# Optimization experiments

Hardware: AMD Instinct MI355X
Metric: run time of the kernel (lower is better)

Reference implementation:

```python
import jax, jax.numpy as jnp
import numpy as np

B, T, C = 2, 2048, 1024
N_HEAD = 16
HEAD_DIM = C // N_HEAD


def setup_inputs() -> dict:
    key = jax.random.key(0)
    k1, k2, k3, k4, k5 = jax.random.split(key, 5)
    s = 1.0 / np.sqrt(C)
    return {
        "x": jax.random.normal(k1, (B, T, C), dtype=jnp.float32),
        "w_attn": jax.random.normal(k2, (C, 3 * C), dtype=jnp.float32) * s,
        "b_attn": jax.random.normal(k3, (3 * C,), dtype=jnp.float32) * 0.02,
        "w_proj": jax.random.normal(k4, (C, C), dtype=jnp.float32) * s,
        "b_proj": jax.random.normal(k5, (C,), dtype=jnp.float32) * 0.02,
    }


def reference(x, w_attn, b_attn, w_proj, b_proj):
    Bx, Tx, Cx = x.shape
    qkv = x @ w_attn + b_attn  # [B, T, 3C]
    q, k, v = jnp.split(qkv, 3, axis=2)
    # [B, H, T, D]
    q = q.reshape(Bx, Tx, N_HEAD, HEAD_DIM).transpose(0, 2, 1, 3)
    k = k.reshape(Bx, Tx, N_HEAD, HEAD_DIM).transpose(0, 2, 1, 3)
    v = v.reshape(Bx, Tx, N_HEAD, HEAD_DIM).transpose(0, 2, 1, 3)
    scale = 1.0 / jnp.sqrt(jnp.asarray(HEAD_DIM, dtype=x.dtype))
    att = jnp.einsum("bhqd,bhkd->bhqk", q, k) * scale  # [B,H,T,T]
    causal = jnp.tril(jnp.ones((Tx, Tx), dtype=bool))
    att = jnp.where(causal[None, None, :, :], att, -jnp.inf)
    att = jax.nn.softmax(att, axis=-1)
    y = jnp.einsum("bhqk,bhkd->bhqd", att, v)  # [B,H,T,D]
    y = y.transpose(0, 2, 1, 3).reshape(Bx, Tx, Cx)
    return y @ w_proj + b_proj
```

## Files before the change

kernel.cpp:

```cpp
#include <hip/hip_runtime.h>
#include <hip/hip_bf16.h>
#include <stdint.h>

#define TT 2048
#define CC 1024
#define NH 16
#define HD 64
#define BT 4096

typedef float f32x4 __attribute__((ext_vector_type(4)));
typedef __bf16 bf16x8 __attribute__((ext_vector_type(8)));
typedef __bf16 bf16x4 __attribute__((ext_vector_type(4)));
typedef short sh4 __attribute__((ext_vector_type(4)));

#define MFMA(a, b, c) __builtin_amdgcn_mfma_f32_16x16x32_bf16((a), (b), (c), 0, 0, 0)
#define MFMA16(a, b, c) __builtin_amdgcn_mfma_f32_16x16x16bf16_1k((a), (b), (c), 0, 0, 0)

__device__ __forceinline__ void gload16(const void* g, void* l) {
    __builtin_amdgcn_global_load_lds(
        (const __attribute__((address_space(1))) void*)g,
        (__attribute__((address_space(3))) void*)l,
        16, 0, 0);
}

__global__ __launch_bounds__(256) void prep(
    const float* __restrict__ x, __bf16* __restrict__ xb,
    const float* __restrict__ wa, __bf16* __restrict__ oa,
    const float* __restrict__ wp, __bf16* __restrict__ op) {
    __shared__ float tile[32][33];
    int b0 = blockIdx.x;
    if (b0 < 1024) {
        int i = b0 * 256 + threadIdx.x;
        const int stride = 1024 * 256;
        const int n4 = BT * CC / 4;
        for (; i < n4; i += stride) {
            float4 v = reinterpret_cast<const float4*>(x)[i];
            bf16x4 o;
            o.x = (__bf16)v.x; o.y = (__bf16)v.y;
            o.z = (__bf16)v.z; o.w = (__bf16)v.w;
            reinterpret_cast<bf16x4*>(xb)[i] = o;
        }
    } else {
        int idx = b0 - 1024;
        int bx = idx & 127, r0 = (idx >> 7) * 32;
        const float* in;
        __bf16* out;
        int C;
        if (bx < 96) { in = wa; out = oa; C = 3072; }
        else         { in = wp; out = op; C = 1024; bx -= 96; }
        int c0 = bx * 32;
        int tx = threadIdx.x & 31, ty = (threadIdx.x >> 5) & 7;
#pragma unroll
        for (int j = 0; j < 32; j += 8)
            tile[ty + j][tx] = in[(size_t)(r0 + ty + j) * C + c0 + tx];
        __syncthreads();
#pragma unroll
        for (int j = 0; j < 32; j += 8)
            out[(size_t)(c0 + ty + j) * 1024 + r0 + tx] = (__bf16)tile[tx][ty + j];
    }
}

template <int MODE, int XPX>
__global__ __launch_bounds__(256) void gemm128(
    const __bf16* __restrict__ A, const __bf16* __restrict__ Bt,
    const float* __restrict__ bias,
    __bf16* __restrict__ oq, __bf16* __restrict__ ok, __bf16* __restrict__ ov,
    float* __restrict__ of, int M, int N, int K) {
    __shared__ __align__(16) __bf16 As[128 * 64];
    __shared__ __align__(16) __bf16 Bs[128 * 64];
    const int tid = threadIdx.x;
    const int w = tid >> 6, lane = tid & 63;
    const int l15 = lane & 15, lg = lane >> 4;
    const int id = blockIdx.x;
    const int jx = id & 7, s = id >> 3;
    const int xcol = jx * XPX + (s % XPX);
    const int yrow = s / XPX;
    const int m0 = yrow * 128, n0 = xcol * 128;
    const int wr = w >> 1, wc = w & 1;

    const f32x4 zero4 = {0.f, 0.f, 0.f, 0.f};
    f32x4 acc[4][4];
#pragma unroll
    for (int m = 0; m < 4; ++m)
#pragma unroll
        for (int n = 0; n < 4; ++n) acc[m][n] = zero4;

    const char* Ab = (const char*)A;
    const char* Bb = (const char*)Bt;
    const size_t rowbytes = (size_t)K * 2;

    for (int kt = 0; kt < K; kt += 64) {
#pragma unroll
        for (int j = 0; j < 4; ++j) {
            int base = (w * 4 + j) * 1024;
            int d0 = base + lane * 16;
            int row = d0 >> 7;
            int colb = d0 & 127;
            int scolb = colb ^ ((row & 7) << 4);
            gload16(Ab + (size_t)(m0 + row) * rowbytes + (size_t)kt * 2 + scolb,
                    (char*)As + base);
            gload16(Bb + (size_t)(n0 + row) * rowbytes + (size_t)kt * 2 + scolb,
                    (char*)Bs + base);
        }
        __syncthreads();
#pragma unroll
        for (int kk = 0; kk < 2; ++kk) {
            bf16x8 af[4], bfr[4];
#pragma unroll
            for (int m = 0; m < 4; ++m) {
                int row = wr * 64 + m * 16 + l15;
                int colb = kk * 64 + lg * 16;
                af[m] = *(const bf16x8*)((const char*)As + row * 128 +
                                         (colb ^ ((row & 7) << 4)));
            }
#pragma unroll
            for (int n = 0; n < 4; ++n) {
                int row = wc * 64 + n * 16 + l15;
                int colb = kk * 64 + lg * 16;
                bfr[n] = *(const bf16x8*)((const char*)Bs + row * 128 +
                                          (colb ^ ((row & 7) << 4)));
            }
#pragma unroll
            for (int m = 0; m < 4; ++m)
#pragma unroll
                for (int n = 0; n < 4; ++n)
                    acc[m][n] = MFMA(af[m], bfr[n], acc[m][n]);
        }
        __syncthreads();
    }

#pragma unroll
    for (int n = 0; n < 4; ++n) {
        int col = n0 + wc * 64 + n * 16 + l15;
        float bs = bias[col];
        if constexpr (MODE == 0) {
            int sec = col >> 10;
            int cc = col & 1023;
            int h = cc >> 6, d = cc & 63;
            if (sec == 2) {
#pragma unroll
                for (int m = 0; m < 4; ++m) {
                    int rowb = m0 + wr * 64 + m * 16 + lg * 4;
                    int bb = rowb >> 11, t = rowb & 2047;
                    bf16x4 pk;
#pragma unroll
                    for (int r = 0; r < 4; ++r) pk[r] = (__bf16)(acc[m][n][r] + bs);
                    size_t base = ((size_t)(bb * NH + h) * HD + d) * (TT * 2);
                    size_t byte = base + (size_t)((t & ~63) * 2 +
                                   (((t & 63) * 2) ^ ((d & 15) << 3)));
                    *(bf16x4*)((char*)ov + byte) = pk;
                }
            } else {
                __bf16* dst = (sec == 0) ? oq : ok;
                float mult = (sec == 0) ? 0.125f * 1.44269504088896340736f : 1.0f;
#pragma unroll
                for (int m = 0; m < 4; ++m) {
                    int rowb = m0 + wr * 64 + m * 16 + lg * 4;
#pragma unroll
                    for (int r = 0; r < 4; ++r) {
                        int row = rowb + r;
                        int bb = row >> 11, t = row & 2047;
                        float val = (acc[m][n][r] + bs) * mult;
                        dst[((size_t)(bb * NH + h) * TT + t) * HD + d] = (__bf16)val;
                    }
                }
            }
        } else {
#pragma unroll
            for (int m = 0; m < 4; ++m) {
                int rowb = m0 + wr * 64 + m * 16 + lg * 4;
#pragma unroll
                for (int r = 0; r < 4; ++r) {
                    int row = rowb + r;
                    of[(size_t)row * N + col] = acc[m][n][r] + bs;
                }
            }
        }
    }
}

__global__ __launch_bounds__(256) void attn_kernel(
    const __bf16* __restrict__ q, const __bf16* __restrict__ k,
    const __bf16* __restrict__ vt, __bf16* __restrict__ y) {
    __shared__ __align__(16) __bf16 Kb[2][64 * 64];
    __shared__ __align__(16) __bf16 Vb[2][64 * 64];

    const int n = blockIdx.x;
    const int batch = n >> 8, a = (n >> 5) & 7;
    const int qt = (batch == 0) ? 31 - a : (batch == 1) ? 16 + a
                 : (batch == 2) ? 15 - a : a;
    const int bh = ((n & 7) << 2) | ((n >> 3) & 3);
    const int tid = threadIdx.x, w = tid >> 6, lane = tid & 63;
    const int l15 = lane & 15, lg = lane >> 4;
    const char* kh = (const char*)(k + (size_t)bh * TT * HD);
    const char* vh = (const char*)(vt + (size_t)bh * HD * TT);
    const __bf16* qh = q + (size_t)bh * TT * HD;
    const int qbw = qt * 64 + w * 16;

    const f32x4 zero4 = {0.f, 0.f, 0.f, 0.f};
    float lrun = 0.f;
    f32x4 oacc[4];
    bf16x8 qf[2];
#pragma unroll
    for (int f = 0; f < 4; ++f) oacc[f] = zero4;
#pragma unroll
    for (int kk = 0; kk < 2; ++kk)
        qf[kk] = *(const bf16x8*)&qh[(size_t)(qbw + l15) * HD + kk * 32 + lg * 8];

    auto stage = [&](int kvb, int buf) {
#pragma unroll
        for (int j = 0; j < 2; ++j) {
            int d0 = ((w * 2 + j) * 64 + lane) * 16;
            int row = d0 >> 7, colb = d0 & 127;
            gload16(kh + (size_t)(kvb + row) * 128 + (colb ^ ((row & 7) << 4)),
                    (char*)Kb[buf] + d0);
            gload16(vh + (size_t)row * (TT * 2) + (size_t)kvb * 2 + colb,
                    (char*)Vb[buf] + d0);
        }
    };

    stage(0, 0);
    __syncthreads();

    for (int g = 0; g <= qt; ++g) {
        const int cur = g & 1;
        if (g < qt) stage((g + 1) * 64, cur ^ 1);
        const int kb = g * 64;

        f32x4 s[4];
#pragma unroll
        for (int kf = 0; kf < 4; ++kf) s[kf] = zero4;
        __builtin_amdgcn_s_setprio(1);
#pragma unroll
        for (int kf = 0; kf < 4; ++kf) {
            int krow = kf * 16 + l15;
            const char* kr = (const char*)Kb[cur] + krow * 128;
            bf16x8 k0 = *(const bf16x8*)(kr + ((lg * 16) ^ ((krow & 7) << 4)));
            bf16x8 k1 = *(const bf16x8*)(kr + ((64 + lg * 16) ^ ((krow & 7) << 4)));
            s[kf] = MFMA(k0, qf[0], s[kf]);
            s[kf] = MFMA(k1, qf[1], s[kf]);
        }
        __builtin_amdgcn_s_setprio(0);
        if (g == qt) {
            const int qq = qbw + l15;
#pragma unroll
            for (int kf = 0; kf < 4; ++kf)
#pragma unroll
                for (int r = 0; r < 4; ++r) {
                    int kk_ = kb + kf * 16 + lg * 4 + r;
                    if (kk_ > qq) s[kf][r] = -1e30f;
                }
        }
        float ss = 0.f;
        sh4 pb[4];
#pragma unroll
        for (int kf = 0; kf < 4; ++kf) {
            bf16x4 pk;
#pragma unroll
            for (int r = 0; r < 4; ++r) {
                float p = exp2f(s[kf][r]);
                pk[r] = (__bf16)p;
                ss += p;
            }
            pb[kf] = __builtin_bit_cast(sh4, pk);
        }
        lrun += ss;
        __builtin_amdgcn_s_setprio(1);
#pragma unroll
        for (int kf = 0; kf < 4; ++kf) {
            int cb = (kf * 32 + lg * 8) ^ (l15 << 3);
#pragma unroll
            for (int f = 0; f < 4; ++f) {
                int vrow = f * 16 + l15;
                bf16x4 va = *(const bf16x4*)((const char*)Vb[cur] + vrow * 128 + cb);
                oacc[f] = MFMA16(__builtin_bit_cast(sh4, va), pb[kf], oacc[f]);
            }
        }
        __builtin_amdgcn_s_setprio(0);
        __syncthreads();
    }

    lrun += __shfl_xor(lrun, 16);
    lrun += __shfl_xor(lrun, 32);
    const int b = bh >> 4, h = bh & 15;
    float inv = 1.0f / lrun;
#pragma unroll
    for (int f = 0; f < 4; ++f) {
        bf16x4 pk;
#pragma unroll
        for (int r = 0; r < 4; ++r) pk[r] = (__bf16)(oacc[f][r] * inv);
        *(bf16x4*)&y[(size_t)(b * TT + qbw + l15) * CC + h * 64 + f * 16 +
                     lg * 4] = pk;
    }
}

extern "C" void kernel_launch(void* const* d_in, const int* in_sizes, int n_in,
                              void* d_out, int out_size, void* d_ws, size_t ws_size,
                              hipStream_t stream) {
    const float* x      = (const float*)d_in[0];
    const float* w_attn = (const float*)d_in[1];
    const float* b_attn = (const float*)d_in[2];
    const float* w_proj = (const float*)d_in[3];
    const float* b_proj = (const float*)d_in[4];
    float* out = (float*)d_out;

    char* ws = (char*)d_ws;
    size_t off = 0;
    auto alloc = [&](size_t bytes) {
        char* p = ws + off;
        off += (bytes + 255) & ~(size_t)255;
        return p;
    };
    __bf16* xb   = (__bf16*)alloc((size_t)BT * CC * 2);
    __bf16* watb = (__bf16*)alloc((size_t)3 * CC * CC * 2);
    __bf16* wptb = (__bf16*)alloc((size_t)CC * CC * 2);
    __bf16* qb   = (__bf16*)alloc((size_t)BT * CC * 2);
    __bf16* kbuf = (__bf16*)alloc((size_t)BT * CC * 2);
    __bf16* vtb  = (__bf16*)alloc((size_t)BT * CC * 2);
    __bf16* yb   = (__bf16*)alloc((size_t)BT * CC * 2);

    prep<<<5120, 256, 0, stream>>>(x, xb, w_attn, watb, w_proj, wptb);

    gemm128<0, 3><<<768, 256, 0, stream>>>(
        xb, watb, b_attn, qb, kbuf, vtb, nullptr, BT, 3 * CC, CC);

    attn_kernel<<<1024, 256, 0, stream>>>(qb, kbuf, vtb, yb);

    gemm128<1, 1><<<256, 256, 0, stream>>>(
        yb, wptb, b_proj, nullptr, nullptr, nullptr, out, BT, CC, CC);
}
```

Baseline: 109.1 us.

## Pair complementary causal query tiles per attention block to share K/V loads

Each attention workgroup now handles two query tiles (qt and 31-qt) of the same head, sharing the staged K/V tiles for the overlapping prefix. The grid halves to 512 blocks and every block does a balanced amount of causal work. This is meant to cut redundant K/V global and LDS traffic and remove load imbalance. In exchange it doubles accumulator register use, which may lower occupancy, and leaves fewer blocks to fill the GPU.

```diff
diff --git a/kernel.cpp b/kernel.cpp
--- a/kernel.cpp
+++ b/kernel.cpp
@@ -186,31 +186,34 @@
     __shared__ __align__(16) __bf16 Vb[2][64 * 64];
 
     const int n = blockIdx.x;
-    const int batch = n >> 8, a = (n >> 5) & 7;
-    const int qt = (batch == 0) ? 31 - a : (batch == 1) ? 16 + a
-                 : (batch == 2) ? 15 - a : a;
+    const int sl = (n >> 5) & 7;
+    const int j = (n < 256) ? (15 - sl) : sl;
+    const int qtA = 15 - j, qtB = 16 + j;
     const int bh = ((n & 7) << 2) | ((n >> 3) & 3);
     const int tid = threadIdx.x, w = tid >> 6, lane = tid & 63;
     const int l15 = lane & 15, lg = lane >> 4;
     const char* kh = (const char*)(k + (size_t)bh * TT * HD);
     const char* vh = (const char*)(vt + (size_t)bh * HD * TT);
     const __bf16* qh = q + (size_t)bh * TT * HD;
-    const int qbw = qt * 64 + w * 16;
+    const int qbwA = qtA * 64 + w * 16;
+    const int qbwB = qtB * 64 + w * 16;
 
     const f32x4 zero4 = {0.f, 0.f, 0.f, 0.f};
-    float lrun = 0.f;
-    f32x4 oacc[4];
-    bf16x8 qf[2];
-#pragma unroll
-    for (int f = 0; f < 4; ++f) oacc[f] = zero4;
-#pragma unroll
-    for (int kk = 0; kk < 2; ++kk)
-        qf[kk] = *(const bf16x8*)&qh[(size_t)(qbw + l15) * HD + kk * 32 + lg * 8];
+    float lrunA = 0.f, lrunB = 0.f;
+    f32x4 oaccA[4], oaccB[4];
+    bf16x8 qfA[2], qfB[2];
+#pragma unroll
+    for (int f = 0; f < 4; ++f) { oaccA[f] = zero4; oaccB[f] = zero4; }
+#pragma unroll
+    for (int kk = 0; kk < 2; ++kk) {
+        qfA[kk] = *(const bf16x8*)&qh[(size_t)(qbwA + l15) * HD + kk * 32 + lg * 8];
+        qfB[kk] = *(const bf16x8*)&qh[(size_t)(qbwB + l15) * HD + kk * 32 + lg * 8];
+    }
 
     auto stage = [&](int kvb, int buf) {
 #pragma unroll
-        for (int j = 0; j < 2; ++j) {
-            int d0 = ((w * 2 + j) * 64 + lane) * 16;
+        for (int jj = 0; jj < 2; ++jj) {
+            int d0 = ((w * 2 + jj) * 64 + lane) * 16;
             int row = d0 >> 7, colb = d0 & 127;
             gload16(kh + (size_t)(kvb + row) * 128 + (colb ^ ((row & 7) << 4)),
                     (char*)Kb[buf] + d0);
@@ -222,74 +225,147 @@
     stage(0, 0);
     __syncthreads();
 
-    for (int g = 0; g <= qt; ++g) {
+    for (int g = 0; g <= qtB; ++g) {
         const int cur = g & 1;
-        if (g < qt) stage((g + 1) * 64, cur ^ 1);
+        if (g < qtB) stage((g + 1) * 64, cur ^ 1);
         const int kb = g * 64;
 
-        f32x4 s[4];
-#pragma unroll
-        for (int kf = 0; kf < 4; ++kf) s[kf] = zero4;
-        __builtin_amdgcn_s_setprio(1);
-#pragma unroll
-        for (int kf = 0; kf < 4; ++kf) {
-            int krow = kf * 16 + l15;
-            const char* kr = (const char*)Kb[cur] + krow * 128;
-            bf16x8 k0 = *(const bf16x8*)(kr + ((lg * 16) ^ ((krow & 7) << 4)));
-            bf16x8 k1 = *(const bf16x8*)(kr + ((64 + lg * 16) ^ ((krow & 7) << 4)));
-            s[kf] = MFMA(k0, qf[0], s[kf]);
-            s[kf] = MFMA(k1, qf[1], s[kf]);
-        }
-        __builtin_amdgcn_s_setprio(0);
-        if (g == qt) {
-            const int qq = qbw + l15;
-#pragma unroll
-            for (int kf = 0; kf < 4; ++kf)
+        if (g <= qtA) {
+            f32x4 sA[4], sB[4];
+#pragma unroll
+            for (int kf = 0; kf < 4; ++kf) { sA[kf] = zero4; sB[kf] = zero4; }
+            __builtin_amdgcn_s_setprio(1);
+#pragma unroll
+            for (int kf = 0; kf < 4; ++kf) {
+                int krow = kf * 16 + l15;
+                const char* kr = (const char*)Kb[cur] + krow * 128;
+                bf16x8 k0 = *(const bf16x8*)(kr + ((lg * 16) ^ ((krow & 7) << 4)));
+                bf16x8 k1 = *(const bf16x8*)(kr + ((64 + lg * 16) ^ ((krow & 7) << 4)));
+                sB[kf] = MFMA(k0, qfB[0], sB[kf]);
+                sB[kf] = MFMA(k1, qfB[1], sB[kf]);
+                sA[kf] = MFMA(k0, qfA[0], sA[kf]);
+                sA[kf] = MFMA(k1, qfA[1], sA[kf]);
+            }
+            __builtin_amdgcn_s_setprio(0);
+            if (g == qtA) {
+                const int qq = qbwA + l15;
+#pragma unroll
+                for (int kf = 0; kf < 4; ++kf)
+#pragma unroll
+                    for (int r = 0; r < 4; ++r) {
+                        int kk_ = kb + kf * 16 + lg * 4 + r;
+                        if (kk_ > qq) sA[kf][r] = -1e30f;
+                    }
+            }
+            sh4 pbA[4], pbB[4];
+            float ssA = 0.f, ssB = 0.f;
+#pragma unroll
+            for (int kf = 0; kf < 4; ++kf) {
+                bf16x4 pkA, pkB;
 #pragma unroll
                 for (int r = 0; r < 4; ++r) {
-                    int kk_ = kb + kf * 16 + lg * 4 + r;
-                    if (kk_ > qq) s[kf][r] = -1e30f;
-                }
-        }
-        float ss = 0.f;
-        sh4 pb[4];
-#pragma unroll
-        for (int kf = 0; kf < 4; ++kf) {
-            bf16x4 pk;
-#pragma unroll
-            for (int r = 0; r < 4; ++r) {
-                float p = exp2f(s[kf][r]);
-                pk[r] = (__bf16)p;
-                ss += p;
-            }
-            pb[kf] = __builtin_bit_cast(sh4, pk);
-        }
-        lrun += ss;
-        __builtin_amdgcn_s_setprio(1);
-#pragma unroll
-        for (int kf = 0; kf < 4; ++kf) {
-            int cb = (kf * 32 + lg * 8) ^ (l15 << 3);
-#pragma unroll
-            for (int f = 0; f < 4; ++f) {
-                int vrow = f * 16 + l15;
-                bf16x4 va = *(const bf16x4*)((const char*)Vb[cur] + vrow * 128 + cb);
-                oacc[f] = MFMA16(__builtin_bit_cast(sh4, va), pb[kf], oacc[f]);
-            }
-        }
-        __builtin_amdgcn_s_setprio(0);
+                    float pB = exp2f(sB[kf][r]);
+                    float pA = exp2f(sA[kf][r]);
+                    pkB[r] = (__bf16)pB;
+                    pkA[r] = (__bf16)pA;
+                    ssB += pB;
+                    ssA += pA;
+                }
+                pbB[kf] = __builtin_bit_cast(sh4, pkB);
+                pbA[kf] = __builtin_bit_cast(sh4, pkA);
+            }
+            lrunA += ssA;
+            lrunB += ssB;
+            __builtin_amdgcn_s_setprio(1);
+#pragma unroll
+            for (int kf = 0; kf < 4; ++kf) {
+                int cb = (kf * 32 + lg * 8) ^ (l15 << 3);
+#pragma unroll
+                for (int f = 0; f < 4; ++f) {
+                    int vrow = f * 16 + l15;
+                    bf16x4 va = *(const bf16x4*)((const char*)Vb[cur] + vrow * 128 + cb);
+                    sh4 vs = __builtin_bit_cast(sh4, va);
+                    oaccB[f] = MFMA16(vs, pbB[kf], oaccB[f]);
+                    oaccA[f] = MFMA16(vs, pbA[kf], oaccA[f]);
+                }
+            }
+            __builtin_amdgcn_s_setprio(0);
+        } else {
+            f32x4 s[4];
+#pragma unroll
+            for (int kf = 0; kf < 4; ++kf) s[kf] = zero4;
+            __builtin_amdgcn_s_setprio(1);
+#pragma unroll
+            for (int kf = 0; kf < 4; ++kf) {
+                int krow = kf * 16 + l15;
+                const char* kr = (const char*)Kb[cur] + krow * 128;
+                bf16x8 k0 = *(const bf16x8*)(kr + ((lg * 16) ^ ((krow & 7) << 4)));
+                bf16x8 k1 = *(const bf16x8*)(kr + ((64 + lg * 16) ^ ((krow & 7) << 4)));
+                s[kf] = MFMA(k0, qfB[0], s[kf]);
+                s[kf] = MFMA(k1, qfB[1], s[kf]);
+            }
+            __builtin_amdgcn_s_setprio(0);
+            if (g == qtB) {
+                const int qq = qbwB + l15;
+#pragma unroll
+                for (int kf = 0; kf < 4; ++kf)
+#pragma unroll
+                    for (int r = 0; r < 4; ++r) {
+                        int kk_ = kb + kf * 16 + lg * 4 + r;
+                        if (kk_ > qq) s[kf][r] = -1e30f;
+                    }
+            }
+            float ss = 0.f;
+            sh4 pb[4];
+#pragma unroll
+            for (int kf = 0; kf < 4; ++kf) {
+                bf16x4 pk;
+#pragma unroll
+                for (int r = 0; r < 4; ++r) {
+                    float p = exp2f(s[kf][r]);
+                    pk[r] = (__bf16)p;
+                    ss += p;
+                }
+                pb[kf] = __builtin_bit_cast(sh4, pk);
+            }
+            lrunB += ss;
+            __builtin_amdgcn_s_setprio(1);
+#pragma unroll
+            for (int kf = 0; kf < 4; ++kf) {
+                int cb = (kf * 32 + lg * 8) ^ (l15 << 3);
+#pragma unroll
+                for (int f = 0; f < 4; ++f) {
+                    int vrow = f * 16 + l15;
+                    bf16x4 va = *(const bf16x4*)((const char*)Vb[cur] + vrow * 128 + cb);
+                    oaccB[f] = MFMA16(__builtin_bit_cast(sh4, va), pb[kf], oaccB[f]);
+                }
+            }
+            __builtin_amdgcn_s_setprio(0);
+        }
         __syncthreads();
     }
 
-    lrun += __shfl_xor(lrun, 16);
-    lrun += __shfl_xor(lrun, 32);
     const int b = bh >> 4, h = bh & 15;
-    float inv = 1.0f / lrun;
+    lrunA += __shfl_xor(lrunA, 16);
+    lrunA += __shfl_xor(lrunA, 32);
+    float invA = 1.0f / lrunA;
 #pragma unroll
     for (int f = 0; f < 4; ++f) {
         bf16x4 pk;
 #pragma unroll
-        for (int r = 0; r < 4; ++r) pk[r] = (__bf16)(oacc[f][r] * inv);
-        *(bf16x4*)&y[(size_t)(b * TT + qbw + l15) * CC + h * 64 + f * 16 +
+        for (int r = 0; r < 4; ++r) pk[r] = (__bf16)(oaccA[f][r] * invA);
+        *(bf16x4*)&y[(size_t)(b * TT + qbwA + l15) * CC + h * 64 + f * 16 +
+                     lg * 4] = pk;
+    }
+    lrunB += __shfl_xor(lrunB, 16);
+    lrunB += __shfl_xor(lrunB, 32);
+    float invB = 1.0f / lrunB;
+#pragma unroll
+    for (int f = 0; f < 4; ++f) {
+        bf16x4 pk;
+#pragma unroll
+        for (int r = 0; r < 4; ++r) pk[r] = (__bf16)(oaccB[f][r] * invB);
+        *(bf16x4*)&y[(size_t)(b * TT + qbwB + l15) * CC + h * 64 + f * 16 +
                      lg * 4] = pk;
     }
 }
@@ -324,7 +400,7 @@
     gemm128<0, 3><<<768, 256, 0, stream>>>(
         xb, watb, b_attn, qb, kbuf, vtb, nullptr, BT, 3 * CC, CC);
 
-    attn_kernel<<<1024, 256, 0, stream>>>(qb, kbuf, vtb, yb);
+    attn_kernel<<<512, 256, 0, stream>>>(qb, kbuf, vtb, yb);
 
     gemm128<1, 1><<<256, 256, 0, stream>>>(
         yb, wptb, b_proj, nullptr, nullptr, nullptr, out, BT, CC, CC);
```

New measurement: 109.1 us. Within noise of the previous version (+0.0%).

## Triple-buffer K/V tiles and software-pipeline QK^T one tile ahead

Applied to the files above, without the earlier changes.

The attention loop moves from double to triple buffering of the K/V tiles in LDS, issuing global loads two iterations ahead. QK^T for the next tile is computed before softmax and PV of the current tile, so MFMA work can overlap the exp/convert phase. The loop barrier becomes an explicit vmcnt(0) wait plus s_barrier. This costs more LDS (48KB per block), which may lower occupancy, and more registers for the extra score tile.

```diff
diff --git a/kernel.cpp b/kernel.cpp
--- a/kernel.cpp
+++ b/kernel.cpp
@@ -182,8 +182,8 @@
 __global__ __launch_bounds__(256) void attn_kernel(
     const __bf16* __restrict__ q, const __bf16* __restrict__ k,
     const __bf16* __restrict__ vt, __bf16* __restrict__ y) {
-    __shared__ __align__(16) __bf16 Kb[2][64 * 64];
-    __shared__ __align__(16) __bf16 Vb[2][64 * 64];
+    __shared__ __align__(16) __bf16 Kb[3][64 * 64];
+    __shared__ __align__(16) __bf16 Vb[3][64 * 64];
 
     const int n = blockIdx.x;
     const int batch = n >> 8, a = (n >> 5) & 7;
@@ -218,37 +218,47 @@
                     (char*)Vb[buf] + d0);
         }
     };
-
-    stage(0, 0);
-    __syncthreads();
-
-    for (int g = 0; g <= qt; ++g) {
-        const int cur = g & 1;
-        if (g < qt) stage((g + 1) * 64, cur ^ 1);
-        const int kb = g * 64;
-
-        f32x4 s[4];
-#pragma unroll
-        for (int kf = 0; kf < 4; ++kf) s[kf] = zero4;
-        __builtin_amdgcn_s_setprio(1);
+    auto qkt = [&](int buf, f32x4 (&sout)[4]) {
+#pragma unroll
+        for (int kf = 0; kf < 4; ++kf) sout[kf] = zero4;
 #pragma unroll
         for (int kf = 0; kf < 4; ++kf) {
             int krow = kf * 16 + l15;
-            const char* kr = (const char*)Kb[cur] + krow * 128;
+            const char* kr = (const char*)Kb[buf] + krow * 128;
             bf16x8 k0 = *(const bf16x8*)(kr + ((lg * 16) ^ ((krow & 7) << 4)));
             bf16x8 k1 = *(const bf16x8*)(kr + ((64 + lg * 16) ^ ((krow & 7) << 4)));
-            s[kf] = MFMA(k0, qf[0], s[kf]);
-            s[kf] = MFMA(k1, qf[1], s[kf]);
-        }
+            sout[kf] = MFMA(k0, qf[0], sout[kf]);
+            sout[kf] = MFMA(k1, qf[1], sout[kf]);
+        }
+    };
+
+    stage(0, 0);
+    if (qt > 0) stage(64, 1);
+    asm volatile("s_waitcnt vmcnt(0)" ::: "memory");
+    __builtin_amdgcn_sched_barrier(0);
+    __builtin_amdgcn_s_barrier();
+
+    f32x4 scur[4];
+    qkt(0, scur);
+
+    for (int g = 0; g <= qt; ++g) {
+        const int cur = g % 3;
+        if (g + 2 <= qt) stage((g + 2) * 64, (g + 2) % 3);
+
+        f32x4 snext[4];
+        __builtin_amdgcn_s_setprio(1);
+        if (g < qt) qkt((g + 1) % 3, snext);
         __builtin_amdgcn_s_setprio(0);
+
         if (g == qt) {
+            const int kb = g * 64;
             const int qq = qbw + l15;
 #pragma unroll
             for (int kf = 0; kf < 4; ++kf)
 #pragma unroll
                 for (int r = 0; r < 4; ++r) {
                     int kk_ = kb + kf * 16 + lg * 4 + r;
-                    if (kk_ > qq) s[kf][r] = -1e30f;
+                    if (kk_ > qq) scur[kf][r] = -1e30f;
                 }
         }
         float ss = 0.f;
@@ -258,7 +268,7 @@
             bf16x4 pk;
 #pragma unroll
             for (int r = 0; r < 4; ++r) {
-                float p = exp2f(s[kf][r]);
+                float p = exp2f(scur[kf][r]);
                 pk[r] = (__bf16)p;
                 ss += p;
             }
@@ -277,7 +287,14 @@
             }
         }
         __builtin_amdgcn_s_setprio(0);
-        __syncthreads();
+
+        if (g < qt) {
+            asm volatile("s_waitcnt vmcnt(0)" ::: "memory");
+            __builtin_amdgcn_sched_barrier(0);
+            __builtin_amdgcn_s_barrier();
+#pragma unroll
+            for (int kf = 0; kf < 4; ++kf) scur[kf] = snext[kf];
+        }
     }
 
     lrun += __shfl_xor(lrun, 16);
```

Result: no change. 108.1 us (-0.9%).
